# Performance work log

Hardware: AMD Instinct MI355X
Metric: run time of the kernel (lower is better)

## Reference

```python
import jax, jax.numpy as jnp
import numpy as np

BS, NQ, DIMS = 4, 6400, 256
NH, NL, NP, NQUEUE = 8, 1, 4, 2


def ms_deform_attn(value, shapes_np, starts_np, loc, attn):
    # value: [B, Nv, H, D]; loc: [B, Nq, H, L, P, 2] in [0,1]; attn: [B, Nq, H, L, P]
    B, Nv, H, D = value.shape
    _, Nq, _, L, P, _ = loc.shape
    out = jnp.zeros((B, H, Nq, D), loc.dtype)
    for l in range(L):
        Hl, Wl = int(shapes_np[l, 0]), int(shapes_np[l, 1])
        s = int(starts_np[l])
        vl = value[:, s:s + Hl * Wl].transpose(0, 2, 1, 3)  # [B,H,HW,D]
        # grid_sample align_corners=False pixel coords
        x = loc[:, :, :, l, :, 0] * Wl - 0.5  # [B,Nq,H,P]
        y = loc[:, :, :, l, :, 1] * Hl - 0.5
        x0 = jnp.floor(x); y0 = jnp.floor(y)
        dx = x - x0; dy = y - y0
        x0i = x0.astype(jnp.int32); y0i = y0.astype(jnp.int32)
        acc = jnp.zeros((B, H, Nq * P, D), loc.dtype)
        corners = [(x0i, y0i, (1 - dx) * (1 - dy)),
                   (x0i + 1, y0i, dx * (1 - dy)),
                   (x0i, y0i + 1, (1 - dx) * dy),
                   (x0i + 1, y0i + 1, dx * dy)]
        for xi, yi, w in corners:
            valid = (xi >= 0) & (xi < Wl) & (yi >= 0) & (yi < Hl)
            idx = jnp.clip(yi, 0, Hl - 1) * Wl + jnp.clip(xi, 0, Wl - 1)  # [B,Nq,H,P]
            idx_t = idx.transpose(0, 2, 1, 3).reshape(B, H, Nq * P, 1)
            g = jnp.take_along_axis(vl, idx_t, axis=2)  # [B,H,Nq*P,D]
            wv = jnp.where(valid, w, 0.0).transpose(0, 2, 1, 3).reshape(B, H, Nq * P, 1)
            acc = acc + g * wv
        acc = acc.reshape(B, H, Nq, P, D)
        wl = attn[:, :, :, l].transpose(0, 2, 1, 3)  # [B,H,Nq,P]
        out = out + jnp.einsum('bhnpd,bhnp->bhnd', acc, wl)
    return out.transpose(0, 2, 1, 3).reshape(B, Nq, H * D)


def setup_inputs() -> dict:
    key = jax.random.key(0)
    ks = jax.random.split(key, 12)
    d2 = DIMS * NQUEUE
    noff = NQUEUE * NH * NL * NP * 2
    nattn = NQUEUE * NH * NL * NP
    sc = 1.0 / np.sqrt(DIMS)
    return {
        'query': jax.random.normal(ks[0], (BS, NQ, DIMS), jnp.float32),
        'voxbev': jax.random.normal(ks[1], (BS, NQ, DIMS), jnp.float32),
        'reference_points': jax.random.uniform(ks[2], (BS * NQUEUE, NQ, NL, 2), jnp.float32),
        'spatial_shapes': jnp.array([[80, 80]], dtype=jnp.int64),
        'level_start_index': jnp.array([0], dtype=jnp.int64),
        'Wv': jax.random.normal(ks[3], (DIMS, DIMS), jnp.float32) * sc,
        'bv': jax.random.normal(ks[4], (DIMS,), jnp.float32) * 0.01,
        'Woff': jax.random.normal(ks[5], (d2, noff), jnp.float32) * (1.0 / np.sqrt(d2)),
        'boff': jax.random.normal(ks[6], (noff,), jnp.float32),
        'Wattn': jax.random.normal(ks[7], (d2, nattn), jnp.float32) * (1.0 / np.sqrt(d2)),
        'battn': jax.random.normal(ks[8], (nattn,), jnp.float32) * 0.01,
        'Wo': jax.random.normal(ks[9], (DIMS, DIMS), jnp.float32) * sc,
        'bo': jax.random.normal(ks[10], (DIMS,), jnp.float32) * 0.01,
    }


def reference(query, voxbev, reference_points, spatial_shapes, level_start_index,
              Wv, bv, Woff, boff, Wattn, battn, Wo, bo):
    bs, nq, dims = query.shape
    shapes_np = np.asarray(spatial_shapes)
    starts_np = np.asarray(level_start_index)
    identity = query
    # value = stack([query, voxbev], 1).reshape(bs*2, nq, dims) -> interleaved [q0,v0,q1,v1,...]
    value = jnp.stack([query, voxbev], 1).reshape(bs * NQUEUE, nq, dims)
    qcat = jnp.concatenate([value[:bs], query], -1)  # [bs, nq, 2*dims]
    v = (value @ Wv + bv).reshape(bs * NQUEUE, nq, NH, dims // NH)
    off = (qcat @ Woff + boff).reshape(bs, nq, NH, NQUEUE, NL, NP, 2)
    attn = (qcat @ Wattn + battn).reshape(bs, nq, NH, NQUEUE, NL * NP)
    attn = jax.nn.softmax(attn, axis=-1).reshape(bs, nq, NH, NQUEUE, NL, NP)
    attn = attn.transpose(0, 3, 1, 2, 4, 5).reshape(bs * NQUEUE, nq, NH, NL, NP)
    off = off.transpose(0, 3, 1, 2, 4, 5, 6).reshape(bs * NQUEUE, nq, NH, NL, NP, 2)
    # offset normalizer: (W, H) per level
    norm = jnp.stack([spatial_shapes[:, 1], spatial_shapes[:, 0]], -1).astype(off.dtype)  # [L,2]
    loc = reference_points[:, :, None, :, None, :] + off / norm[None, None, None, :, None, :]
    out = ms_deform_attn(v, shapes_np, starts_np, loc, attn)  # [bs*2, nq, dims]
    out = out.reshape(bs, NQUEUE, nq, dims).mean(1)  # mean over queue
    out = out @ Wo + bo
    return out + identity  # dropout is identity in eval
```

## Files before the change

kernel.cpp:

```cpp
#include <hip/hip_runtime.h>
#include <hip/hip_bf16.h>

#define BS   4
#define NQ   6400
#define DIMS 256
#define NH   8
#define NP   4
#define GW   80
#define GH   80

typedef __hip_bfloat16 bf16;
typedef unsigned short ushort;
typedef __attribute__((ext_vector_type(8))) short short8;
typedef __attribute__((ext_vector_type(4))) float floatx4;

union bfu { bf16 h; ushort s; };
__device__ __forceinline__ ushort f2bs(float x) { bfu u; u.h = __float2bfloat16(x); return u.s; }
__device__ __forceinline__ float bs2f(ushort s) { return __uint_as_float(((unsigned)s) << 16); }
__device__ __forceinline__ float ldin(const void* p, size_t i, int isf) {
    return isf ? ((const float*)p)[i] : bs2f(((const ushort*)p)[i]);
}

__device__ __forceinline__ void gl_lds16(const void* gsrc, void* ldst) {
    __builtin_amdgcn_global_load_lds(
        (const __attribute__((address_space(1))) unsigned int*)gsrc,
        (__attribute__((address_space(3))) unsigned int*)ldst,
        16, 0, 0);
}

__device__ __forceinline__ int self_detect(const ushort* __restrict__ q, int tid) {
    int bad = 0;
    const uint4 u0 = ((const uint4*)q)[tid * 2];
    const uint4 u1 = ((const uint4*)q)[tid * 2 + 1];
    const unsigned w[8] = { u0.x, u0.y, u0.z, u0.w, u1.x, u1.y, u1.z, u1.w };
    #pragma unroll
    for (int j = 0; j < 8; ++j) {
        if (((w[j] >> 7)  & 0xFF) > 160) bad = 1;
        if (((w[j] >> 23) & 0xFF) > 160) bad = 1;
    }
    return __any(bad) ? 1 : 0;
}

__global__ __launch_bounds__(256) void prep_k(
    const void* __restrict__ Wv, const void* __restrict__ bv,
    const void* __restrict__ Woff, const void* __restrict__ boff,
    const void* __restrict__ Wattn, const void* __restrict__ battn,
    const void* __restrict__ Wo, const void* __restrict__ bo,
    int* __restrict__ flagp,
    ushort* __restrict__ WvT, ushort* __restrict__ WoaT, ushort* __restrict__ WoT,
    float* __restrict__ biasv, float* __restrict__ biasoa, float* __restrict__ biaso,
    const void* __restrict__ query, const void* __restrict__ voxbev,
    uint4* __restrict__ qb, uint4* __restrict__ vbv)
{
    const int tid = threadIdx.x;
    const int isf = self_detect((const ushort*)query, tid);
    const int bid = blockIdx.x;
    if (bid == 0 && tid == 0) *flagp = isf;
    if (bid < 899) {
        const int i = bid * 256 + tid;
        const int n1 = 256 * 256, n2 = n1 + 192 * 512, n3 = n2 + 256 * 256;
        const int n4 = n3 + 256, n5 = n4 + 192, n6 = n5 + 256;
        if (i < n1) {
            int n = i >> 8, k = i & 255;
            WvT[i] = f2bs(ldin(Wv, (size_t)k * 256 + n, isf));
        } else if (i < n2) {
            int j = i - n1, n = j >> 9, k = j & 511;
            float v = (n < 128) ? ldin(Woff, (size_t)k * 128 + n, isf)
                                : ldin(Wattn, (size_t)k * 64 + (n - 128), isf);
            WoaT[j] = f2bs(v);
        } else if (i < n3) {
            int j = i - n2, n = j >> 8, k = j & 255;
            WoT[j] = f2bs(ldin(Wo, (size_t)k * 256 + n, isf));
        } else if (i < n4) {
            biasv[i - n3] = ldin(bv, i - n3, isf);
        } else if (i < n5) {
            int j = i - n4;
            biasoa[j] = (j < 128) ? ldin(boff, j, isf) : ldin(battn, j - 128, isf);
        } else if (i < n6) {
            biaso[i - n5] = ldin(bo, i - n5, isf);
        }
    } else {
        if (isf == 0) return;
        const int t = (bid - 899) * 256 + tid;
        const int half = 819200;
        const void* src = (t < half) ? query : voxbev;
        uint4* dst = (t < half) ? qb : vbv;
        const int j = (t < half) ? t : t - half;
        const float4* s = (const float4*)src + (size_t)j * 2;
        float4 a = s[0], b = s[1];
        uint4 o;
        o.x = ((unsigned)f2bs(a.y) << 16) | f2bs(a.x);
        o.y = ((unsigned)f2bs(a.w) << 16) | f2bs(a.z);
        o.z = ((unsigned)f2bs(b.y) << 16) | f2bs(b.x);
        o.w = ((unsigned)f2bs(b.w) << 16) | f2bs(b.z);
        dst[j] = o;
    }
}

enum { A_VAL = 0, A_QCAT = 1, A_PLAIN = 2 };
enum { O_BF16 = 0, O_FINAL = 1, O_VPERM = 2, O_OAPERM = 3 };

#define BKS  128
#define ABYT (128 * 256)
#define BBYT (64 * 256)
#define CST  67
#define SMEMB (ABYT + BBYT)

template <int AMODE, int OMODE, int KTOT, int NX, int MG>
__device__ __forceinline__ void pgemm_body(
    const int F, char* smem,
    const ushort* __restrict__ Apl, const ushort* __restrict__ BT,
    const float* __restrict__ biasf, void* __restrict__ C,
    const void* __restrict__ query_raw, const void* __restrict__ voxbev_raw,
    const ushort* __restrict__ qb, const ushort* __restrict__ vbv,
    const int isf)
{
    constexpr int N = NX * 64;
    constexpr int NT = KTOT / BKS;
    char* abuf = smem;
    char* bbuf = smem + ABYT;
    float* cbf = (float*)smem;

    const int xcd = F & 7, l = F >> 3;
    const int n = l % NX;
    const int mg = (l / NX) * 8 + xcd;
    if (mg >= MG) return;
    const int bm = mg * 128, bn = n * 64;

    const int tid = threadIdx.x;
    const int lane = tid & 63, wv = tid >> 6;
    const int wm = wv * 32;
    const int fr = lane & 15;
    const int srow = lane >> 4;
    const int sslot = lane & 15;

    const ushort* qsrc = isf ? qb  : (const ushort*)query_raw;
    const ushort* vsrc = isf ? vbv : (const ushort*)voxbev_raw;
    const ushort* aph[2] = { nullptr, nullptr };
    if (AMODE == A_PLAIN) {
        aph[0] = Apl + (size_t)bm * DIMS;
    } else {
        const int b = bm / NQ, q0 = bm - (bm / NQ) * NQ;
        aph[0] = ((b & 1) ? vsrc : qsrc) + (size_t)((b >> 1) * NQ + q0) * DIMS;
        if (AMODE == A_QCAT) aph[1] = qsrc + (size_t)(b * NQ + q0) * DIMS;
    }

    floatx4 acc[2][4] = {};

    #pragma unroll
    for (int t = 0; t < NT; ++t) {
        if (t > 0) __syncthreads();
        #pragma unroll
        for (int c8 = 0; c8 < 8; ++c8) {
            const int c = wv * 8 + c8;
            const int row = c * 4 + srow;
            const int g = sslot ^ (row & 15);
            const int k = t * BKS + g * 8;
            const ushort* gp;
            if (AMODE == A_QCAT && KTOT == 512)
                gp = aph[k >> 8] + (size_t)row * DIMS + (k & 255);
            else
                gp = aph[0] + (size_t)row * DIMS + k;
            gl_lds16(gp, abuf + c * 1024);
        }
        #pragma unroll
        for (int c4 = 0; c4 < 4; ++c4) {
            const int c = wv * 4 + c4;
            const int row = c * 4 + srow;
            const int g = sslot ^ (row & 15);
            gl_lds16(&BT[(size_t)(bn + row) * KTOT + t * BKS + g * 8],
                     bbuf + c * 1024);
        }
        asm volatile("s_waitcnt vmcnt(0)" ::: "memory");
        __syncthreads();

        #pragma unroll
        for (int k0 = 0; k0 < BKS; k0 += 32) {
            const int gl = (k0 >> 3) + (lane >> 4);
            short8 af[2], bf[4];
            #pragma unroll
            for (int mt = 0; mt < 2; ++mt)
                af[mt] = *(const short8*)(abuf + (wm + mt * 16 + fr) * 256
                                               + ((gl ^ fr) * 16));
            #pragma unroll
            for (int nt = 0; nt < 4; ++nt)
                bf[nt] = *(const short8*)(bbuf + (nt * 16 + fr) * 256
                                               + ((gl ^ fr) * 16));
            #pragma unroll
            for (int mt = 0; mt < 2; ++mt)
                #pragma unroll
                for (int nt = 0; nt < 4; ++nt)
                    acc[mt][nt] = __builtin_amdgcn_mfma_f32_16x16x32_bf16(
                        af[mt], bf[nt], acc[mt][nt], 0, 0, 0);
        }
    }

    __syncthreads();
    const int col = lane & 15, rq = (lane >> 4) * 4;
    #pragma unroll
    for (int mt = 0; mt < 2; ++mt)
        #pragma unroll
        for (int nt = 0; nt < 4; ++nt)
            #pragma unroll
            for (int r = 0; r < 4; ++r)
                cbf[(wm + mt * 16 + rq + r) * CST + nt * 16 + col] = acc[mt][nt][r];
    __syncthreads();

    if (OMODE == O_FINAL && isf) {
        const int r16 = tid >> 4, cc = tid & 15;
        #pragma unroll
        for (int it = 0; it < 8; ++it) {
            const int lr = it * 16 + r16;
            const size_t g = (size_t)(bm + lr);
            float4 x = *(const float4*)&cbf[lr * CST + cc * 4];
            const ushort* rs = qsrc + g * DIMS + bn + cc * 4;
            x.x += biasf[bn + cc * 4 + 0] + bs2f(rs[0]);
            x.y += biasf[bn + cc * 4 + 1] + bs2f(rs[1]);
            x.z += biasf[bn + cc * 4 + 2] + bs2f(rs[2]);
            x.w += biasf[bn + cc * 4 + 3] + bs2f(rs[3]);
            *(float4*)((float*)C + g * N + bn + cc * 4) = x;
        }
    } else {
        const int r8 = tid >> 3, c8 = tid & 7;
        #pragma unroll
        for (int it = 0; it < 4; ++it) {
            const int lr = it * 32 + r8;
            const size_t g = (size_t)(bm + lr);
            float4 x0 = *(const float4*)&cbf[lr * CST + c8 * 8];
            float4 x1 = *(const float4*)&cbf[lr * CST + c8 * 8 + 4];
            float xs[8] = { x0.x, x0.y, x0.z, x0.w, x1.x, x1.y, x1.z, x1.w };
            #pragma unroll
            for (int e = 0; e < 8; ++e) xs[e] += biasf[bn + c8 * 8 + e];
            if (OMODE == O_FINAL) {
                const ushort* rs = qsrc + g * DIMS + bn + c8 * 8;
                #pragma unroll
                for (int e = 0; e < 8; ++e) xs[e] += bs2f(rs[e]);
            }
            uint4 o;
            o.x = ((unsigned)f2bs(xs[1]) << 16) | f2bs(xs[0]);
            o.y = ((unsigned)f2bs(xs[3]) << 16) | f2bs(xs[2]);
            o.z = ((unsigned)f2bs(xs[5]) << 16) | f2bs(xs[4]);
            o.w = ((unsigned)f2bs(xs[7]) << 16) | f2bs(xs[6]);
            ushort* dstp;
            if (OMODE == O_VPERM) {
                const int cc = bn + c8 * 8;
                const int s = (int)(g / NQ), qq = (int)(g % NQ);
                dstp = (ushort*)C + ((size_t)(s * 8 + (cc >> 5)) * NQ + qq) * 32
                                  + (cc & 31);
            } else if (OMODE == O_OAPERM) {
                const int cc = bn + c8 * 8;
                const int bb = (int)(g / NQ), qq = (int)(g % NQ);
                int hh, off;
                if (cc < 128) { hh = cc >> 4; off = cc & 15; }
                else          { hh = (cc - 128) >> 3; off = 16; }
                dstp = (ushort*)C + ((size_t)(bb * 8 + hh) * NQ + qq) * 24 + off;
            } else {
                dstp = (ushort*)C + g * N + bn + c8 * 8;
            }
            *(uint4*)dstp = o;
        }
    }
}

__global__ __launch_bounds__(256) void gemm12_k(
    const ushort* __restrict__ WvT, const float* __restrict__ biasv,
    ushort* __restrict__ v_ws,
    const ushort* __restrict__ WoaT, const float* __restrict__ biasoa,
    ushort* __restrict__ offraw,
    const void* __restrict__ query_raw, const void* __restrict__ voxbev_raw,
    const ushort* __restrict__ qb, const ushort* __restrict__ vbv,
    const int* __restrict__ flagp)
{
    __shared__ __align__(16) char smem[SMEMB];
    const int isf = *flagp;
    const int bid = blockIdx.x;
    if (bid < 1600) {
        pgemm_body<A_VAL, O_VPERM, 256, 4, 400>(bid, smem,
            nullptr, WvT, biasv, (void*)v_ws, query_raw, voxbev_raw, qb, vbv, isf);
    } else {
        pgemm_body<A_QCAT, O_OAPERM, 512, 3, 200>(bid - 1600, smem,
            nullptr, WoaT, biasoa, (void*)offraw, query_raw, voxbev_raw, qb, vbv, isf);
    }
}

__global__ __launch_bounds__(256) void gemm4_k(
    const ushort* __restrict__ Apl, const ushort* __restrict__ BT,
    const float* __restrict__ biasf, void* __restrict__ C,
    const void* __restrict__ query_raw, const void* __restrict__ voxbev_raw,
    const ushort* __restrict__ qb, const ushort* __restrict__ vbv,
    const int* __restrict__ flagp)
{
    __shared__ __align__(16) char smem[SMEMB];
    const int isf = *flagp;
    pgemm_body<A_PLAIN, O_FINAL, 256, 4, 200>(blockIdx.x, smem,
        Apl, BT, biasf, C, query_raw, voxbev_raw, qb, vbv, isf);
}

__global__ __launch_bounds__(256) void sample_k(
    const ushort* __restrict__ v,
    const ushort* __restrict__ offp,
    const void* __restrict__ refpts,
    const int* __restrict__ flagp,
    ushort* __restrict__ sampled)
{
    const int isf = *flagp;
    __shared__ int   sidx[64][2][17];
    __shared__ float swt [64][2][17];
    const int tid = threadIdx.x;
    const int j = blockIdx.x;
    const int h = j & 7;
    const int k = j >> 3;
    const int b = k / 100;
    const int q0 = (k % 100) * 64;

    if (tid < 128) {
        const int lq = tid >> 1, queue = tid & 1;
        const int q = q0 + lq;
        const ushort* rec = offp + ((size_t)(b * 8 + h) * NQ + q) * 24;
        const ushort* al = rec + 16 + queue * 4;
        float l0 = bs2f(al[0]), l1 = bs2f(al[1]), l2 = bs2f(al[2]), l3 = bs2f(al[3]);
        float mx = fmaxf(fmaxf(l0, l1), fmaxf(l2, l3));
        float e0 = __expf(l0 - mx), e1 = __expf(l1 - mx);
        float e2 = __expf(l2 - mx), e3 = __expf(l3 - mx);
        float inv = 0.5f / (e0 + e1 + e2 + e3);
        const int bq = b * 2 + queue;
        const float rx = ldin(refpts, ((size_t)bq * NQ + q) * 2 + 0, isf);
        const float ry = ldin(refpts, ((size_t)bq * NQ + q) * 2 + 1, isf);
        const ushort* od = rec + queue * 8;
        float ww[4] = { e0 * inv, e1 * inv, e2 * inv, e3 * inv };
        #pragma unroll
        for (int p = 0; p < NP; ++p) {
            const float x = rx * (float)GW + bs2f(od[p * 2 + 0]) - 0.5f;
            const float y = ry * (float)GH + bs2f(od[p * 2 + 1]) - 0.5f;
            const float x0f = floorf(x), y0f = floorf(y);
            const float dx = x - x0f, dy = y - y0f;
            const int x0 = (int)x0f, y0 = (int)y0f;
            const float wp = ww[p];
            const float cw4[4] = { wp * (1.0f - dx) * (1.0f - dy),
                                   wp * dx * (1.0f - dy),
                                   wp * (1.0f - dx) * dy,
                                   wp * dx * dy };
            #pragma unroll
            for (int c = 0; c < 4; ++c) {
                const int xs = x0 + (c & 1), ys = y0 + (c >> 1);
                const bool ok = (unsigned)xs < (unsigned)GW && (unsigned)ys < (unsigned)GH;
                const int xi = min(max(xs, 0), GW - 1);
                const int yi = min(max(ys, 0), GH - 1);
                sidx[lq][queue][p * 4 + c] = yi * GW + xi;
                swt [lq][queue][p * 4 + c] = ok ? cw4[c] : 0.0f;
            }
        }
    }
    __syncthreads();

    const int lq = tid >> 2, d8 = tid & 3;
    const int q = q0 + lq;
    float a[8] = {};
    #pragma unroll
    for (int queue = 0; queue < 2; ++queue) {
        const ushort* vb = v + (((size_t)(b * 2 + queue) * 8 + h) * NQ) * 32 + d8 * 8;
        #pragma unroll
        for (int hf = 0; hf < 2; ++hf) {
            uint4 g[8];
            #pragma unroll
            for (int u = 0; u < 8; ++u) {
                const int ci = sidx[lq][queue][hf * 8 + u];
                g[u] = *(const uint4*)&vb[(size_t)ci * 32];
            }
            __builtin_amdgcn_sched_barrier(0);
            #pragma unroll
            for (int u = 0; u < 8; ++u) {
                const float cw = swt[lq][queue][hf * 8 + u];
                a[0] += cw * bs2f((ushort)g[u].x); a[1] += cw * bs2f((ushort)(g[u].x >> 16));
                a[2] += cw * bs2f((ushort)g[u].y); a[3] += cw * bs2f((ushort)(g[u].y >> 16));
                a[4] += cw * bs2f((ushort)g[u].z); a[5] += cw * bs2f((ushort)(g[u].z >> 16));
                a[6] += cw * bs2f((ushort)g[u].w); a[7] += cw * bs2f((ushort)(g[u].w >> 16));
            }
        }
    }
    uint4 o;
    o.x = ((unsigned)f2bs(a[1]) << 16) | f2bs(a[0]);
    o.y = ((unsigned)f2bs(a[3]) << 16) | f2bs(a[2]);
    o.z = ((unsigned)f2bs(a[5]) << 16) | f2bs(a[4]);
    o.w = ((unsigned)f2bs(a[7]) << 16) | f2bs(a[6]);
    *(uint4*)&sampled[((size_t)b * NQ + q) * DIMS + h * 32 + d8 * 8] = o;
}

extern "C" void kernel_launch(void* const* d_in, const int* in_sizes, int n_in,
                              void* d_out, int out_size, void* d_ws, size_t ws_size,
                              hipStream_t stream)
{
    const void* query  = d_in[0];
    const void* voxbev = d_in[1];
    const void* refpts = d_in[2];
    const void* Wv   = d_in[5];  const void* bv    = d_in[6];
    const void* Woff = d_in[7];  const void* boff  = d_in[8];
    const void* Wattn= d_in[9];  const void* battn = d_in[10];
    const void* Wo   = d_in[11]; const void* bo    = d_in[12];

    char* p = (char*)d_ws;
    int* flag = (int*)p;             p += 256;
    ushort* WvT  = (ushort*)p;       p += 256 * 256 * 2;
    ushort* WoaT = (ushort*)p;       p += 192 * 512 * 2;
    ushort* WoT  = (ushort*)p;       p += 256 * 256 * 2;
    float* biasv  = (float*)p;       p += 1024;
    float* biasoa = (float*)p;       p += 1024;
    float* biaso  = (float*)p;       p += 1024;
    ushort* qb   = (ushort*)p;       p += (size_t)BS * NQ * DIMS * 2;
    ushort* vbv  = (ushort*)p;       p += (size_t)BS * NQ * DIMS * 2;
    ushort* v_ws = (ushort*)p;       p += (size_t)2 * BS * NQ * DIMS * 2;
    ushort* offraw = (ushort*)p;     p += (size_t)BS * NQ * 192 * 2;
    ushort* sampled = (ushort*)p;

    prep_k<<<7299, 256, 0, stream>>>(Wv, bv, Woff, boff, Wattn, battn, Wo, bo,
                                     flag, WvT, WoaT, WoT, biasv, biasoa, biaso,
                                     query, voxbev, (uint4*)qb, (uint4*)vbv);

    gemm12_k<<<2200, 256, 0, stream>>>(WvT, biasv, v_ws, WoaT, biasoa, offraw,
                                       query, voxbev, qb, vbv, flag);

    sample_k<<<3200, 256, 0, stream>>>(v_ws, offraw, refpts, flag, sampled);

    gemm4_k<<<800, 256, 0, stream>>>(sampled, WoT, biaso, d_out,
                                     query, voxbev, qb, vbv, flag);
}
```

Measured before the change: 182.7 us.

## Shrink GEMM K-tile to 64 and split epilogue to cut LDS for occupancy

Reduces the GEMM K-step from 128 to 64, halving the A/B LDS staging buffers and reworking the XOR swizzle to fit 8 slots per row. The epilogue is split into two 64-row halves so the C staging buffer fits in the smaller shared memory, and launch bounds request 6 waves per SIMD. The goal is more resident blocks per CU to hide global load latency, in exchange for twice as many barriers and K iterations and an extra epilogue sync round.

Measured after the change: 190.6 us. 1.04x slower.

```diff
diff --git a/kernel.cpp b/kernel.cpp
--- a/kernel.cpp
+++ b/kernel.cpp
@@ -100,9 +100,8 @@
 enum { A_VAL = 0, A_QCAT = 1, A_PLAIN = 2 };
 enum { O_BF16 = 0, O_FINAL = 1, O_VPERM = 2, O_OAPERM = 3 };
 
-#define BKS  128
-#define ABYT (128 * 256)
-#define BBYT (64 * 256)
+#define ABYT 16384
+#define BBYT 8192
 #define CST  67
 #define SMEMB (ABYT + BBYT)
 
@@ -116,9 +115,7 @@
     const int isf)
 {
     constexpr int N = NX * 64;
-    constexpr int NT = KTOT / BKS;
-    char* abuf = smem;
-    char* bbuf = smem + ABYT;
+    constexpr int NT = KTOT / 64;
     float* cbf = (float*)smem;
 
     const int xcd = F & 7, l = F >> 3;
@@ -131,8 +128,9 @@
     const int lane = tid & 63, wv = tid >> 6;
     const int wm = wv * 32;
     const int fr = lane & 15;
-    const int srow = lane >> 4;
-    const int sslot = lane & 15;
+    const int lrow = lane >> 3;
+    const int lslot = lane & 7;
+    const int sg = lslot ^ lrow;
 
     const ushort* qsrc = isf ? qb  : (const ushort*)query_raw;
     const ushort* vsrc = isf ? vbv : (const ushort*)voxbev_raw;
@@ -151,41 +149,40 @@
     for (int t = 0; t < NT; ++t) {
         if (t > 0) __syncthreads();
         #pragma unroll
-        for (int c8 = 0; c8 < 8; ++c8) {
-            const int c = wv * 8 + c8;
-            const int row = c * 4 + srow;
-            const int g = sslot ^ (row & 15);
-            const int k = t * BKS + g * 8;
+        for (int c4 = 0; c4 < 4; ++c4) {
+            const int c = wv * 4 + c4;
+            const int row = c * 8 + lrow;
+            const int k = t * 64 + sg * 8;
             const ushort* gp;
             if (AMODE == A_QCAT && KTOT == 512)
                 gp = aph[k >> 8] + (size_t)row * DIMS + (k & 255);
             else
                 gp = aph[0] + (size_t)row * DIMS + k;
-            gl_lds16(gp, abuf + c * 1024);
+            gl_lds16(gp, smem + c * 1024);
         }
         #pragma unroll
-        for (int c4 = 0; c4 < 4; ++c4) {
-            const int c = wv * 4 + c4;
-            const int row = c * 4 + srow;
-            const int g = sslot ^ (row & 15);
-            gl_lds16(&BT[(size_t)(bn + row) * KTOT + t * BKS + g * 8],
-                     bbuf + c * 1024);
+        for (int c2 = 0; c2 < 2; ++c2) {
+            const int c = wv * 2 + c2;
+            const int row = c * 8 + lrow;
+            gl_lds16(&BT[(size_t)(bn + row) * KTOT + t * 64 + sg * 8],
+                     smem + ABYT + c * 1024);
         }
         asm volatile("s_waitcnt vmcnt(0)" ::: "memory");
         __syncthreads();
 
+        const short* acur = (const short*)smem;
+        const short* bcur = (const short*)(smem + ABYT);
         #pragma unroll
-        for (int k0 = 0; k0 < BKS; k0 += 32) {
+        for (int k0 = 0; k0 < 64; k0 += 32) {
             const int gl = (k0 >> 3) + (lane >> 4);
+            const int sl = gl ^ (fr & 7);
             short8 af[2], bf[4];
             #pragma unroll
             for (int mt = 0; mt < 2; ++mt)
-                af[mt] = *(const short8*)(abuf + (wm + mt * 16 + fr) * 256
-                                               + ((gl ^ fr) * 16));
+                af[mt] = *(const short8*)&acur[(wm + mt * 16 + fr) * 64 + sl * 8];
             #pragma unroll
             for (int nt = 0; nt < 4; ++nt)
-                bf[nt] = *(const short8*)(bbuf + (nt * 16 + fr) * 256
-                                               + ((gl ^ fr) * 16));
+                bf[nt] = *(const short8*)&bcur[(nt * 16 + fr) * 64 + sl * 8];
             #pragma unroll
             for (int mt = 0; mt < 2; ++mt)
                 #pragma unroll
@@ -195,74 +192,81 @@
         }
     }
 
-    __syncthreads();
     const int col = lane & 15, rq = (lane >> 4) * 4;
+    const int lbase = wm & 63;
     #pragma unroll
-    for (int mt = 0; mt < 2; ++mt)
-        #pragma unroll
-        for (int nt = 0; nt < 4; ++nt)
-            #pragma unroll
-            for (int r = 0; r < 4; ++r)
-                cbf[(wm + mt * 16 + rq + r) * CST + nt * 16 + col] = acc[mt][nt][r];
-    __syncthreads();
-
-    if (OMODE == O_FINAL && isf) {
-        const int r16 = tid >> 4, cc = tid & 15;
-        #pragma unroll
-        for (int it = 0; it < 8; ++it) {
-            const int lr = it * 16 + r16;
-            const size_t g = (size_t)(bm + lr);
-            float4 x = *(const float4*)&cbf[lr * CST + cc * 4];
-            const ushort* rs = qsrc + g * DIMS + bn + cc * 4;
-            x.x += biasf[bn + cc * 4 + 0] + bs2f(rs[0]);
-            x.y += biasf[bn + cc * 4 + 1] + bs2f(rs[1]);
-            x.z += biasf[bn + cc * 4 + 2] + bs2f(rs[2]);
-            x.w += biasf[bn + cc * 4 + 3] + bs2f(rs[3]);
-            *(float4*)((float*)C + g * N + bn + cc * 4) = x;
-        }
-    } else {
-        const int r8 = tid >> 3, c8 = tid & 7;
-        #pragma unroll
-        for (int it = 0; it < 4; ++it) {
-            const int lr = it * 32 + r8;
-            const size_t g = (size_t)(bm + lr);
-            float4 x0 = *(const float4*)&cbf[lr * CST + c8 * 8];
-            float4 x1 = *(const float4*)&cbf[lr * CST + c8 * 8 + 4];
-            float xs[8] = { x0.x, x0.y, x0.z, x0.w, x1.x, x1.y, x1.z, x1.w };
-            #pragma unroll
-            for (int e = 0; e < 8; ++e) xs[e] += biasf[bn + c8 * 8 + e];
-            if (OMODE == O_FINAL) {
-                const ushort* rs = qsrc + g * DIMS + bn + c8 * 8;
+    for (int half = 0; half < 2; ++half) {
+        __syncthreads();
+        if ((wv >> 1) == half) {
+            #pragma unroll
+            for (int mt = 0; mt < 2; ++mt)
                 #pragma unroll
-                for (int e = 0; e < 8; ++e) xs[e] += bs2f(rs[e]);
+                for (int nt = 0; nt < 4; ++nt)
+                    #pragma unroll
+                    for (int r = 0; r < 4; ++r)
+                        cbf[(lbase + mt * 16 + rq + r) * CST + nt * 16 + col] =
+                            acc[mt][nt][r];
+        }
+        __syncthreads();
+
+        if (OMODE == O_FINAL && isf) {
+            const int r16 = tid >> 4, cc = tid & 15;
+            #pragma unroll
+            for (int it = 0; it < 4; ++it) {
+                const int lr = it * 16 + r16;
+                const size_t g = (size_t)(bm + half * 64 + lr);
+                float4 x = *(const float4*)&cbf[lr * CST + cc * 4];
+                const ushort* rs = qsrc + g * DIMS + bn + cc * 4;
+                x.x += biasf[bn + cc * 4 + 0] + bs2f(rs[0]);
+                x.y += biasf[bn + cc * 4 + 1] + bs2f(rs[1]);
+                x.z += biasf[bn + cc * 4 + 2] + bs2f(rs[2]);
+                x.w += biasf[bn + cc * 4 + 3] + bs2f(rs[3]);
+                *(float4*)((float*)C + g * N + bn + cc * 4) = x;
             }
-            uint4 o;
-            o.x = ((unsigned)f2bs(xs[1]) << 16) | f2bs(xs[0]);
-            o.y = ((unsigned)f2bs(xs[3]) << 16) | f2bs(xs[2]);
-            o.z = ((unsigned)f2bs(xs[5]) << 16) | f2bs(xs[4]);
-            o.w = ((unsigned)f2bs(xs[7]) << 16) | f2bs(xs[6]);
-            ushort* dstp;
-            if (OMODE == O_VPERM) {
-                const int cc = bn + c8 * 8;
-                const int s = (int)(g / NQ), qq = (int)(g % NQ);
-                dstp = (ushort*)C + ((size_t)(s * 8 + (cc >> 5)) * NQ + qq) * 32
-                                  + (cc & 31);
-            } else if (OMODE == O_OAPERM) {
-                const int cc = bn + c8 * 8;
-                const int bb = (int)(g / NQ), qq = (int)(g % NQ);
-                int hh, off;
-                if (cc < 128) { hh = cc >> 4; off = cc & 15; }
-                else          { hh = (cc - 128) >> 3; off = 16; }
-                dstp = (ushort*)C + ((size_t)(bb * 8 + hh) * NQ + qq) * 24 + off;
-            } else {
-                dstp = (ushort*)C + g * N + bn + c8 * 8;
+        } else {
+            const int r8 = tid >> 3, c8 = tid & 7;
+            #pragma unroll
+            for (int it = 0; it < 2; ++it) {
+                const int lr = it * 32 + r8;
+                const size_t g = (size_t)(bm + half * 64 + lr);
+                float4 x0 = *(const float4*)&cbf[lr * CST + c8 * 8];
+                float4 x1 = *(const float4*)&cbf[lr * CST + c8 * 8 + 4];
+                float xs[8] = { x0.x, x0.y, x0.z, x0.w, x1.x, x1.y, x1.z, x1.w };
+                #pragma unroll
+                for (int e = 0; e < 8; ++e) xs[e] += biasf[bn + c8 * 8 + e];
+                if (OMODE == O_FINAL) {
+                    const ushort* rs = qsrc + g * DIMS + bn + c8 * 8;
+                    #pragma unroll
+                    for (int e = 0; e < 8; ++e) xs[e] += bs2f(rs[e]);
+                }
+                uint4 o;
+                o.x = ((unsigned)f2bs(xs[1]) << 16) | f2bs(xs[0]);
+                o.y = ((unsigned)f2bs(xs[3]) << 16) | f2bs(xs[2]);
+                o.z = ((unsigned)f2bs(xs[5]) << 16) | f2bs(xs[4]);
+                o.w = ((unsigned)f2bs(xs[7]) << 16) | f2bs(xs[6]);
+                ushort* dstp;
+                if (OMODE == O_VPERM) {
+                    const int cc = bn + c8 * 8;
+                    const int s = (int)(g / NQ), qq = (int)(g % NQ);
+                    dstp = (ushort*)C + ((size_t)(s * 8 + (cc >> 5)) * NQ + qq) * 32
+                                      + (cc & 31);
+                } else if (OMODE == O_OAPERM) {
+                    const int cc = bn + c8 * 8;
+                    const int bb = (int)(g / NQ), qq = (int)(g % NQ);
+                    int hh, off;
+                    if (cc < 128) { hh = cc >> 4; off = cc & 15; }
+                    else          { hh = (cc - 128) >> 3; off = 16; }
+                    dstp = (ushort*)C + ((size_t)(bb * 8 + hh) * NQ + qq) * 24 + off;
+                } else {
+                    dstp = (ushort*)C + g * N + bn + c8 * 8;
+                }
+                *(uint4*)dstp = o;
             }
-            *(uint4*)dstp = o;
-        }
-    }
-}
-
-__global__ __launch_bounds__(256) void gemm12_k(
+        }
+    }
+}
+
+__global__ __launch_bounds__(256, 6) void gemm12_k(
     const ushort* __restrict__ WvT, const float* __restrict__ biasv,
     ushort* __restrict__ v_ws,
     const ushort* __restrict__ WoaT, const float* __restrict__ biasoa,
@@ -283,7 +287,7 @@
     }
 }
 
-__global__ __launch_bounds__(256) void gemm4_k(
+__global__ __launch_bounds__(256, 6) void gemm4_k(
     const ushort* __restrict__ Apl, const ushort* __restrict__ BT,
     const float* __restrict__ biasf, void* __restrict__ C,
     const void* __restrict__ query_raw, const void* __restrict__ voxbev_raw,
```
